# Optimization experiments

Measured on AMD Instinct MI355X. Metric: run time of the kernel, lower is better.

## Reference

```python
import jax, jax.numpy as jnp
import numpy as np

N = 100000
E = 1600000
DIN = 128
H = 64
OUT_CLAMP = 10.0


def setup_inputs() -> dict:
    key = jax.random.key(0)
    ks = jax.random.split(key, 8)
    x = jax.random.normal(ks[0], (N, DIN), dtype=jnp.float32)
    edge_index = jax.random.randint(ks[1], (2, E), 0, N, dtype=jnp.int64)
    edge_weight = jax.random.uniform(ks[2], (E,), dtype=jnp.float32)
    # learned params (glorot-ish scale)
    W1 = jax.random.normal(ks[3], (DIN, H), dtype=jnp.float32) / np.sqrt(DIN)
    b1 = jnp.zeros((H,), dtype=jnp.float32)
    W2 = jax.random.normal(ks[4], (H, H), dtype=jnp.float32) / np.sqrt(H)
    b2 = jnp.zeros((H,), dtype=jnp.float32)
    fc_w = jax.random.normal(ks[5], (H, 1), dtype=jnp.float32) / np.sqrt(H)
    fc_b = jnp.zeros((1,), dtype=jnp.float32)
    return {"x": x, "edge_index": edge_index, "edge_weight": edge_weight,
            "W1": W1, "b1": b1, "W2": W2, "b2": b2, "fc_w": fc_w, "fc_b": fc_b}


def _gcn_conv(h, src, dst, norm, W, b, n_nodes):
    # h: [N, Fin] -> [N, Fout]. PyG GCNConv: linear, gather at source,
    # scale by symmetric norm, scatter-add at target, add bias.
    hw = h @ W                                   # [N, Fout]
    msg = hw[src] * norm[:, None]                # [E+N, Fout]
    out = jax.ops.segment_sum(msg, dst, num_segments=n_nodes)
    return out + b


def _gcn_norm(edge_index, edge_weight, n_nodes):
    # add self-loops with weight 1, compute deg^-1/2 symmetric norm
    loop = jnp.arange(n_nodes, dtype=edge_index.dtype)
    src = jnp.concatenate([edge_index[0], loop])
    dst = jnp.concatenate([edge_index[1], loop])
    ew = jnp.concatenate([edge_weight, jnp.ones((n_nodes,), edge_weight.dtype)])
    deg = jax.ops.segment_sum(ew, dst, num_segments=n_nodes)
    dis = jnp.where(deg > 0, jax.lax.rsqrt(jnp.maximum(deg, 1e-12)), 0.0)
    norm = dis[src] * ew * dis[dst]
    return src, dst, norm


def reference(x, edge_index, edge_weight, W1, b1, W2, b2, fc_w, fc_b):
    src, dst, norm = _gcn_norm(edge_index, edge_weight, N)
    h = _gcn_conv(x, src, dst, norm, W1, b1, N)
    h = _gcn_conv(h, src, dst, norm, W2, b2, N)
    out = h @ fc_w + fc_b                        # [N, 1]
    out = jnp.clip(out, 0.0, OUT_CLAMP)
    return jnp.round(out)
```

## Files before the change

### kernel.cpp

```cpp
#include <hip/hip_runtime.h>

#define DIN 128
#define BINW 128
#define BINSHIFT 7
#define NB_MAX 1024
#define CHUNK 8192


__global__ void precompute_kernel(const float* __restrict__ W1, const float* __restrict__ b1,
                                  const float* __restrict__ W2, const float* __restrict__ b2,
                                  const float* __restrict__ fcw, const float* __restrict__ fcb,
                                  double* __restrict__ w1f, double* __restrict__ cvals) {
    const int t = threadIdx.x;
    __shared__ double sw2f[64];
    if (t < 64) {
        double s = 0.0;
        for (int j = 0; j < 64; j++) s += (double)W2[t * 64 + j] * (double)fcw[j];
        sw2f[t] = s;
    }
    __syncthreads();
    if (t < 128) {
        double s = 0.0;
        for (int j = 0; j < 64; j++) s += (double)W1[t * 64 + j] * sw2f[j];
        w1f[t] = s;
    }
    if (t == 128) {
        double c1 = 0.0, c0 = (double)fcb[0];
        for (int j = 0; j < 64; j++) {
            c1 += (double)b1[j] * sw2f[j];
            c0 += (double)b2[j] * (double)fcw[j];
        }
        cvals[0] = c0;
        cvals[1] = c1;
    }
}

__global__ __launch_bounds__(256) void hist_gemv_kernel(
        const int* __restrict__ dst, const float* __restrict__ X,
        const double* __restrict__ w1f, unsigned* __restrict__ histT,
        double2* __restrict__ pk1, int n, int e, int nb, int hblk) {
    __shared__ unsigned cnt[NB_MAX];
    const int blk = blockIdx.x;
    const int t = threadIdx.x;
    if (blk < hblk) {
        for (int b = t; b < nb; b += 256) cnt[b] = 0u;
        __syncthreads();
        const long base = (long)blk * CHUNK;
        for (int k = 0; k < CHUNK / 256; k++) {
            long i = base + k * 256 + t;
            if (i < e) atomicAdd(&cnt[dst[i] >> BINSHIFT], 1u);
        }
        __syncthreads();
        for (int b = t; b < nb; b += 256)
            histT[(long)blk * nb + b] = cnt[b];
        return;
    }
    long g = (long)(blk - hblk) * 256 + t;
    int row = (int)(g >> 6);
    int lane = (int)(g & 63);
    if (row >= n) return;
    float2 x = *(const float2*)(X + (long)row * DIN + 2 * lane);
    double v = (double)x.x * w1f[2 * lane] + (double)x.y * w1f[2 * lane + 1];
#pragma unroll
    for (int off = 32; off > 0; off >>= 1) v += __shfl_down(v, off, 64);
    if (lane == 0) pk1[row].x = v;
}

__global__ __launch_bounds__(256) void binscan_kernel(
        const unsigned* __restrict__ histT, unsigned* __restrict__ chunkOfsT,
        unsigned* __restrict__ binCnt, int nb, int hblk) {
    int gw = (int)((blockIdx.x * 256 + threadIdx.x) >> 6);
    int l = threadIdx.x & 63;
    if (gw >= nb) return;
    unsigned carry = 0u;
    for (int c0 = 0; c0 < hblk; c0 += 64) {
        int c = c0 + l;
        unsigned v = (c < hblk) ? histT[(long)c * nb + gw] : 0u;
        unsigned s = v;
#pragma unroll
        for (int off = 1; off < 64; off <<= 1) {
            unsigned u = __shfl_up(s, off, 64);
            if (l >= off) s += u;
        }
        if (c < hblk) chunkOfsT[(long)c * nb + gw] = carry + s - v;
        carry += (unsigned)__shfl((int)s, 63, 64);
    }
    if (l == 0) binCnt[gw] = carry;
}

__global__ void scan_kernel(const unsigned* __restrict__ binCnt,
                            unsigned* __restrict__ binBase, int nb) {
    __shared__ unsigned part[256];
    const int t = threadIdx.x;
    unsigned loc[4];
    unsigned s = 0;
#pragma unroll
    for (int k = 0; k < 4; k++) {
        int idx = t * 4 + k;
        unsigned v = (idx < nb) ? binCnt[idx] : 0u;
        loc[k] = s;
        s += v;
    }
    part[t] = s;
    __syncthreads();
    if (t == 0) {
        unsigned run = 0;
        for (int j = 0; j < 256; j++) { unsigned v = part[j]; part[j] = run; run += v; }
    }
    __syncthreads();
    unsigned p = part[t];
#pragma unroll
    for (int k = 0; k < 4; k++) {
        int idx = t * 4 + k;
        if (idx < nb) binBase[idx] = p + loc[k];
    }
    if (t == 255) binBase[nb] = p + s;
}

__global__ __launch_bounds__(1024) void binscatter_kernel(
        const int* __restrict__ src, const int* __restrict__ dst,
        const float* __restrict__ ew, const unsigned* __restrict__ binBase,
        const unsigned* __restrict__ chunkOfsT,
        uint2* __restrict__ binned, int e, int nb) {
    __shared__ unsigned cnt[NB_MAX];
    __shared__ unsigned sbase[NB_MAX];
    const int c = blockIdx.x;
    const int t = threadIdx.x;
    for (int b = t; b < nb; b += 1024) {
        cnt[b] = 0u;
        sbase[b] = binBase[b] + chunkOfsT[(long)c * nb + b];
    }
    __syncthreads();
    const long base = (long)c * CHUNK;
#pragma unroll
    for (int k = 0; k < CHUNK / 1024; k++) {
        long i = base + k * 1024 + t;
        if (i < e) {
            int d = dst[i];
            int b = d >> BINSHIFT;
            unsigned p = sbase[b] + atomicAdd(&cnt[b], 1u);
            binned[p] = uint2{(unsigned)src[i] | ((unsigned)(d & (BINW - 1)) << 20),
                              __float_as_uint(ew[i])};
        }
    }
}

__global__ __launch_bounds__(256) void setup_kernel(
        const uint2* __restrict__ binned, const unsigned* __restrict__ binBase,
        const double* __restrict__ cvals,
        double2* __restrict__ pk1, double2* __restrict__ pk2, int n) {
    __shared__ float ws[BINW];
    const int b = blockIdx.x;
    const int t = threadIdx.x;
    if (t < BINW) ws[t] = 0.0f;
    __syncthreads();
    const unsigned s0 = binBase[b], s1 = binBase[b + 1];
    for (unsigned i = s0 + t; i < s1; i += 256) {
        uint2 v = binned[i];
        atomicAdd(&ws[v.x >> 20], __uint_as_float(v.y));
    }
    __syncthreads();
    if (t < BINW) {
        int node = b * BINW + t;
        if (node < n) {
            float d = 1.0f + ws[t];
            float di = (d > 0.0f) ? (1.0f / sqrtf(fmaxf(d, 1e-12f))) : 0.0f;
            double qv = pk1[node].x;
            pk1[node] = double2{qv, (double)di};
            pk2[node] = double2{cvals[1] + (double)(di * di) * qv, (double)di};
        }
    }
}

__global__ __launch_bounds__(256) void spmv1_kernel(
        const uint2* __restrict__ binned, const unsigned* __restrict__ binBase,
        const double2* __restrict__ pk1, double2* __restrict__ pk2, int n) {
    __shared__ double acc[BINW];
    const int b = blockIdx.x;
    const int t = threadIdx.x;
    if (t < BINW) acc[t] = 0.0;
    __syncthreads();
    const unsigned s0 = binBase[b], s1 = binBase[b + 1];
    for (unsigned tile = s0; tile < s1; tile += 1024) {
        uint2 ee[4];
        double2 aa[4];
        bool ok[4];
#pragma unroll
        for (int k = 0; k < 4; k++) {
            unsigned idx = tile + t + k * 256u;
            ok[k] = (idx < s1);
            if (ok[k]) ee[k] = binned[idx];
        }
#pragma unroll
        for (int k = 0; k < 4; k++)
            if (ok[k]) aa[k] = pk1[ee[k].x & 0xFFFFFu];
#pragma unroll
        for (int k = 0; k < 4; k++)
            if (ok[k]) {
                float nm = (float)aa[k].y * __uint_as_float(ee[k].y);
                atomicAdd(&acc[ee[k].x >> 20], (double)nm * aa[k].x);
            }
    }
    __syncthreads();
    if (t < BINW) {
        int node = b * BINW + t;
        if (node < n) {
            double2 me = pk2[node];
            pk2[node].x = me.x + me.y * acc[t];
        }
    }
}

__global__ __launch_bounds__(256) void spmv2_head_kernel(
        const uint2* __restrict__ binned, const unsigned* __restrict__ binBase,
        const double2* __restrict__ pk2, const double* __restrict__ cvals,
        float* __restrict__ out, int n) {
    __shared__ double acc[BINW];
    const int b = blockIdx.x;
    const int t = threadIdx.x;
    if (t < BINW) acc[t] = 0.0;
    __syncthreads();
    const unsigned s0 = binBase[b], s1 = binBase[b + 1];
    for (unsigned tile = s0; tile < s1; tile += 1024) {
        uint2 ee[4];
        double2 aa[4];
        bool ok[4];
#pragma unroll
        for (int k = 0; k < 4; k++) {
            unsigned idx = tile + t + k * 256u;
            ok[k] = (idx < s1);
            if (ok[k]) ee[k] = binned[idx];
        }
#pragma unroll
        for (int k = 0; k < 4; k++)
            if (ok[k]) aa[k] = pk2[ee[k].x & 0xFFFFFu];
#pragma unroll
        for (int k = 0; k < 4; k++)
            if (ok[k]) {
                float nm = (float)aa[k].y * __uint_as_float(ee[k].y);
                atomicAdd(&acc[ee[k].x >> 20], (double)nm * aa[k].x);
            }
    }
    __syncthreads();
    if (t < BINW) {
        int node = b * BINW + t;
        if (node < n) {
            double2 me = pk2[node];
            float di = (float)me.y;
            double u = cvals[0] + (double)(di * di) * me.x + me.y * acc[t];
            float o = (float)u;
            o = fminf(fmaxf(o, 0.0f), 10.0f);
            out[node] = rintf(o);
        }
    }
}

extern "C" void kernel_launch(void* const* d_in, const int* in_sizes, int n_in,
                              void* d_out, int out_size, void* d_ws, size_t ws_size,
                              hipStream_t stream) {
    const float* x   = (const float*)d_in[0];
    const int*   eix = (const int*)d_in[1];
    const float* ew  = (const float*)d_in[2];
    const float* W1  = (const float*)d_in[3];
    const float* b1  = (const float*)d_in[4];
    const float* W2  = (const float*)d_in[5];
    const float* b2  = (const float*)d_in[6];
    const float* fcw = (const float*)d_in[7];
    const float* fcb = (const float*)d_in[8];
    float* out = (float*)d_out;

    const int n = in_sizes[0] / DIN;
    const int e = in_sizes[2];
    const int* src = eix;
    const int* dst = eix + e;
    const int nb = (n + BINW - 1) / BINW;
    const int hblk = (e + CHUNK - 1) / CHUNK;

    auto al = [](size_t v) { return (v + 63) & ~(size_t)63; };
    double* ws = (double*)d_ws;
    size_t o = 0;
    double*   w1f     = ws + o; o += al(DIN);
    double*   cvals   = ws + o; o += al(2);
    double2*  pk1     = (double2*)(ws + o); o += al((size_t)n * 2);
    double2*  pk2     = (double2*)(ws + o); o += al((size_t)n * 2);
    unsigned* binCnt  = (unsigned*)(ws + o); o += al(((size_t)nb + 1) / 2);
    unsigned* binBase = (unsigned*)(ws + o); o += al(((size_t)nb + 2) / 2);
    unsigned* histT   = (unsigned*)(ws + o); o += al(((size_t)nb * hblk + 1) / 2);
    unsigned* chunkOfsT = (unsigned*)(ws + o); o += al(((size_t)nb * hblk + 1) / 2);
    uint2*    binned  = (uint2*)(ws + o);

    const int gemvblk = (n + 3) / 4;
    const int bsblk = (nb * 64 + 255) / 256;

    precompute_kernel<<<1, 256, 0, stream>>>(W1, b1, W2, b2, fcw, fcb, w1f, cvals);
    hist_gemv_kernel<<<hblk + gemvblk, 256, 0, stream>>>(dst, x, w1f, histT,
                                                         pk1, n, e, nb, hblk);
    binscan_kernel<<<bsblk, 256, 0, stream>>>(histT, chunkOfsT, binCnt, nb, hblk);
    scan_kernel<<<1, 256, 0, stream>>>(binCnt, binBase, nb);
    binscatter_kernel<<<hblk, 1024, 0, stream>>>(src, dst, ew, binBase, chunkOfsT,
                                                 binned, e, nb);
    setup_kernel<<<nb, 256, 0, stream>>>(binned, binBase, cvals, pk1, pk2, n);
    spmv1_kernel<<<nb, 256, 0, stream>>>(binned, binBase, pk1, pk2, n);
    spmv2_head_kernel<<<nb, 256, 0, stream>>>(binned, binBase, pk2, cvals, out, n);
}
```

Baseline: 191.4 us.

## Pre-scale gather vectors by source norm and widen SpMV tile unroll

Instead of gathering a double2 (value, deg^-1/2) per edge and multiplying by the source norm inside the SpMV, the setup and spmv1 kernels now store pre-scaled per-node doubles (di*q and di*t). The gathers therefore touch 8 bytes per edge instead of 16, and the per-edge float multiply goes away. The destination norm is applied once per node at the end. The SpMV loops also process 8 edges per thread per tile instead of 4 for more memory-level parallelism, which costs more registers and slightly changes rounding order in the norm products.

```diff
diff --git a/kernel.cpp b/kernel.cpp
--- a/kernel.cpp
+++ b/kernel.cpp
@@ -38,7 +38,7 @@
 __global__ __launch_bounds__(256) void hist_gemv_kernel(
         const int* __restrict__ dst, const float* __restrict__ X,
         const double* __restrict__ w1f, unsigned* __restrict__ histT,
-        double2* __restrict__ pk1, int n, int e, int nb, int hblk) {
+        double* __restrict__ q, int n, int e, int nb, int hblk) {
     __shared__ unsigned cnt[NB_MAX];
     const int blk = blockIdx.x;
     const int t = threadIdx.x;
@@ -63,7 +63,7 @@
     double v = (double)x.x * w1f[2 * lane] + (double)x.y * w1f[2 * lane + 1];
 #pragma unroll
     for (int off = 32; off > 0; off >>= 1) v += __shfl_down(v, off, 64);
-    if (lane == 0) pk1[row].x = v;
+    if (lane == 0) q[row] = v;
 }
 
 __global__ __launch_bounds__(256) void binscan_kernel(
@@ -147,8 +147,9 @@
 
 __global__ __launch_bounds__(256) void setup_kernel(
         const uint2* __restrict__ binned, const unsigned* __restrict__ binBase,
-        const double* __restrict__ cvals,
-        double2* __restrict__ pk1, double2* __restrict__ pk2, int n) {
+        const double* __restrict__ cvals, const double* __restrict__ q,
+        float* __restrict__ disA, double* __restrict__ v1,
+        double* __restrict__ tpart, int n) {
     __shared__ float ws[BINW];
     const int b = blockIdx.x;
     const int t = threadIdx.x;
@@ -165,89 +166,88 @@
         if (node < n) {
             float d = 1.0f + ws[t];
             float di = (d > 0.0f) ? (1.0f / sqrtf(fmaxf(d, 1e-12f))) : 0.0f;
-            double qv = pk1[node].x;
-            pk1[node] = double2{qv, (double)di};
-            pk2[node] = double2{cvals[1] + (double)(di * di) * qv, (double)di};
+            double qv = q[node];
+            disA[node] = di;
+            v1[node] = (double)di * qv;
+            tpart[node] = cvals[1] + (double)(di * di) * qv;
         }
     }
 }
 
 __global__ __launch_bounds__(256) void spmv1_kernel(
         const uint2* __restrict__ binned, const unsigned* __restrict__ binBase,
-        const double2* __restrict__ pk1, double2* __restrict__ pk2, int n) {
+        const double* __restrict__ v1, const float* __restrict__ disA,
+        const double* __restrict__ tpart, double* __restrict__ v2, int n) {
     __shared__ double acc[BINW];
     const int b = blockIdx.x;
     const int t = threadIdx.x;
     if (t < BINW) acc[t] = 0.0;
     __syncthreads();
     const unsigned s0 = binBase[b], s1 = binBase[b + 1];
-    for (unsigned tile = s0; tile < s1; tile += 1024) {
-        uint2 ee[4];
-        double2 aa[4];
-        bool ok[4];
-#pragma unroll
-        for (int k = 0; k < 4; k++) {
+    for (unsigned tile = s0; tile < s1; tile += 2048) {
+        uint2 ee[8];
+        double vv[8];
+        bool ok[8];
+#pragma unroll
+        for (int k = 0; k < 8; k++) {
             unsigned idx = tile + t + k * 256u;
             ok[k] = (idx < s1);
             if (ok[k]) ee[k] = binned[idx];
         }
 #pragma unroll
-        for (int k = 0; k < 4; k++)
-            if (ok[k]) aa[k] = pk1[ee[k].x & 0xFFFFFu];
-#pragma unroll
-        for (int k = 0; k < 4; k++)
-            if (ok[k]) {
-                float nm = (float)aa[k].y * __uint_as_float(ee[k].y);
-                atomicAdd(&acc[ee[k].x >> 20], (double)nm * aa[k].x);
-            }
+        for (int k = 0; k < 8; k++)
+            if (ok[k]) vv[k] = v1[ee[k].x & 0xFFFFFu];
+#pragma unroll
+        for (int k = 0; k < 8; k++)
+            if (ok[k])
+                atomicAdd(&acc[ee[k].x >> 20],
+                          (double)__uint_as_float(ee[k].y) * vv[k]);
     }
     __syncthreads();
     if (t < BINW) {
         int node = b * BINW + t;
         if (node < n) {
-            double2 me = pk2[node];
-            pk2[node].x = me.x + me.y * acc[t];
+            double di = (double)disA[node];
+            double tv = tpart[node] + di * acc[t];
+            v2[node] = di * tv;
         }
     }
 }
 
 __global__ __launch_bounds__(256) void spmv2_head_kernel(
         const uint2* __restrict__ binned, const unsigned* __restrict__ binBase,
-        const double2* __restrict__ pk2, const double* __restrict__ cvals,
-        float* __restrict__ out, int n) {
+        const double* __restrict__ v2, const float* __restrict__ disA,
+        const double* __restrict__ cvals, float* __restrict__ out, int n) {
     __shared__ double acc[BINW];
     const int b = blockIdx.x;
     const int t = threadIdx.x;
     if (t < BINW) acc[t] = 0.0;
     __syncthreads();
     const unsigned s0 = binBase[b], s1 = binBase[b + 1];
-    for (unsigned tile = s0; tile < s1; tile += 1024) {
-        uint2 ee[4];
-        double2 aa[4];
-        bool ok[4];
-#pragma unroll
-        for (int k = 0; k < 4; k++) {
+    for (unsigned tile = s0; tile < s1; tile += 2048) {
+        uint2 ee[8];
+        double vv[8];
+        bool ok[8];
+#pragma unroll
+        for (int k = 0; k < 8; k++) {
             unsigned idx = tile + t + k * 256u;
             ok[k] = (idx < s1);
             if (ok[k]) ee[k] = binned[idx];
         }
 #pragma unroll
-        for (int k = 0; k < 4; k++)
-            if (ok[k]) aa[k] = pk2[ee[k].x & 0xFFFFFu];
-#pragma unroll
-        for (int k = 0; k < 4; k++)
-            if (ok[k]) {
-                float nm = (float)aa[k].y * __uint_as_float(ee[k].y);
-                atomicAdd(&acc[ee[k].x >> 20], (double)nm * aa[k].x);
-            }
+        for (int k = 0; k < 8; k++)
+            if (ok[k]) vv[k] = v2[ee[k].x & 0xFFFFFu];
+#pragma unroll
+        for (int k = 0; k < 8; k++)
+            if (ok[k])
+                atomicAdd(&acc[ee[k].x >> 20],
+                          (double)__uint_as_float(ee[k].y) * vv[k]);
     }
     __syncthreads();
     if (t < BINW) {
         int node = b * BINW + t;
         if (node < n) {
-            double2 me = pk2[node];
-            float di = (float)me.y;
-            double u = cvals[0] + (double)(di * di) * me.x + me.y * acc[t];
+            double u = cvals[0] + (double)disA[node] * (v2[node] + acc[t]);
             float o = (float)u;
             o = fminf(fmaxf(o, 0.0f), 10.0f);
             out[node] = rintf(o);
@@ -281,8 +281,11 @@
     size_t o = 0;
     double*   w1f     = ws + o; o += al(DIN);
     double*   cvals   = ws + o; o += al(2);
-    double2*  pk1     = (double2*)(ws + o); o += al((size_t)n * 2);
-    double2*  pk2     = (double2*)(ws + o); o += al((size_t)n * 2);
+    double*   q       = ws + o; o += al((size_t)n);
+    double*   tpart   = ws + o; o += al((size_t)n);
+    double*   v1      = ws + o; o += al((size_t)n);
+    double*   v2      = ws + o; o += al((size_t)n);
+    float*    disA    = (float*)(ws + o);    o += al(((size_t)n + 1) / 2);
     unsigned* binCnt  = (unsigned*)(ws + o); o += al(((size_t)nb + 1) / 2);
     unsigned* binBase = (unsigned*)(ws + o); o += al(((size_t)nb + 2) / 2);
     unsigned* histT   = (unsigned*)(ws + o); o += al(((size_t)nb * hblk + 1) / 2);
@@ -294,12 +297,14 @@
 
     precompute_kernel<<<1, 256, 0, stream>>>(W1, b1, W2, b2, fcw, fcb, w1f, cvals);
     hist_gemv_kernel<<<hblk + gemvblk, 256, 0, stream>>>(dst, x, w1f, histT,
-                                                         pk1, n, e, nb, hblk);
+                                                         q, n, e, nb, hblk);
     binscan_kernel<<<bsblk, 256, 0, stream>>>(histT, chunkOfsT, binCnt, nb, hblk);
     scan_kernel<<<1, 256, 0, stream>>>(binCnt, binBase, nb);
     binscatter_kernel<<<hblk, 1024, 0, stream>>>(src, dst, ew, binBase, chunkOfsT,
                                                  binned, e, nb);
-    setup_kernel<<<nb, 256, 0, stream>>>(binned, binBase, cvals, pk1, pk2, n);
-    spmv1_kernel<<<nb, 256, 0, stream>>>(binned, binBase, pk1, pk2, n);
-    spmv2_head_kernel<<<nb, 256, 0, stream>>>(binned, binBase, pk2, cvals, out, n);
-}
+    setup_kernel<<<nb, 256, 0, stream>>>(binned, binBase, cvals, q, disA, v1,
+                                         tpart, n);
+    spmv1_kernel<<<nb, 256, 0, stream>>>(binned, binBase, v1, disA, tpart, v2, n);
+    spmv2_head_kernel<<<nb, 256, 0, stream>>>(binned, binBase, v2, disA, cvals,
+                                              out, n);
+}
```

After: 191.1 us. About the same (-0.2%).
